# Optimization experiments

Hardware: AMD Instinct MI355X
Metric: run time of the kernel (lower is better)

## Reference

```python
import jax, jax.numpy as jnp
import numpy as np

EMBED_DIM = 256
NUM_EMBED = 1024
COMMIT_COST = 0.25


def setup_inputs() -> dict:
    key = jax.random.key(0)
    kx, kc = jax.random.split(key)
    x = jax.random.normal(kx, (64, 32, 32, EMBED_DIM), dtype=jnp.float32)
    codebook = jax.random.normal(kc, (NUM_EMBED, EMBED_DIM), dtype=jnp.float32)
    return {"x": x, "codebook": codebook}


def reference(x, codebook):
    # flatten to [N, D]
    flat_x = x.reshape(-1, EMBED_DIM)
    distances = (
        jnp.sum(flat_x ** 2, axis=1, keepdims=True)
        + jnp.sum(codebook ** 2, axis=1)
        - 2.0 * jnp.matmul(flat_x, codebook.T)
    )
    encoding_indices = jnp.argmin(distances, axis=1)  # [N]
    quantized = codebook[encoding_indices].reshape(x.shape)
    # losses (detach semantics via stop_gradient)
    q_latent_loss = jnp.mean((quantized - jax.lax.stop_gradient(x)) ** 2)
    e_latent_loss = jnp.mean((x - jax.lax.stop_gradient(quantized)) ** 2)
    loss = q_latent_loss + COMMIT_COST * e_latent_loss
    # straight-through estimator
    quantized = x + jax.lax.stop_gradient(quantized - x)
    return (quantized, loss)
```

## Files before the change

kernel.cpp:

```cpp
#include <hip/hip_runtime.h>

#define D 256
#define K 1024
#define NVEC 65536
#define ROWS 64
#define GROUPC 256
#define NG (K / GROUPC)
#define NKB (D / 32)
#define MARGIN 0.5f
#define MAXC 12
#define MAXP (ROWS * MAXC)

typedef __attribute__((ext_vector_type(8))) __bf16 bf16x8;
typedef __attribute__((ext_vector_type(4))) float floatx4;

__device__ inline unsigned short f2bf(float f) {
    unsigned int u = __float_as_uint(f);
    unsigned int r = u + 0x7fffu + ((u >> 16) & 1u);
    return (unsigned short)(r >> 16);
}
__device__ inline unsigned int fkey(float f) {
    unsigned int b = __float_as_uint(f);
    return (b & 0x80000000u) ? ~b : (b | 0x80000000u);
}
__device__ inline float unfkey(unsigned int k) {
    unsigned int b = (k & 0x80000000u) ? (k & 0x7fffffffu) : ~k;
    return __uint_as_float(b);
}


__global__ void vq_prep(const float* __restrict__ cb, float* __restrict__ cnorm,
                        unsigned short* __restrict__ cbf, float* __restrict__ lossAcc) {
    const int c = blockIdx.x;
    const int l = threadIdx.x;
    float4 v = *(const float4*)&cb[c * D + l * 4];
    float s = v.x * v.x + v.y * v.y + v.z * v.z + v.w * v.w;
#pragma unroll
    for (int off = 32; off > 0; off >>= 1) s += __shfl_down(s, off, 64);
    if (l == 0) cnorm[c] = s;
    const int g = c >> 8, w = (c >> 6) & 3, j = (c >> 4) & 3, col = c & 15;
    const int kb = l >> 3, quad = (l >> 1) & 3, h = (l & 1) * 4;
    const int S = ((g * 8 + kb) * 4 + w) * 4 + j;
    *(ushort4*)(cbf + (size_t)S * 512 + (quad * 16 + col) * 8 + h) =
        make_ushort4(f2bf(v.x), f2bf(v.y), f2bf(v.z), f2bf(v.w));
    if (c == 0 && l == 0) *lossAcc = 0.f;
}

__global__ __launch_bounds__(256, 4) void vq_fused(
        const float* __restrict__ x, const float* __restrict__ cb,
        const unsigned short* __restrict__ cbf, const float* __restrict__ cnorm,
        float* __restrict__ lossAcc, float* __restrict__ out)
{
    __shared__ __align__(16) unsigned short xs[ROWS * D];
    __shared__ unsigned int rowMinU[ROWS];
    __shared__ unsigned long long rowBest[ROWS];
    __shared__ int ccnt[ROWS];
    __shared__ int cand[ROWS][MAXC];
    __shared__ int pairs[MAXP];
    __shared__ int pcnt;
    __shared__ int widx[ROWS];
    __shared__ float wsum[4];

    const int tid = threadIdx.x;
    const int wave = tid >> 6;
    const int lane = tid & 63;
    const int quad = lane >> 4;
    const int col  = lane & 15;
    const int rowBase = blockIdx.x * ROWS;
    const float* xblk = x + (size_t)rowBase * D;

    if (tid < ROWS) { rowMinU[tid] = 0xFFFFFFFFu; rowBest[tid] = ~0ull; ccnt[tid] = 0; }
    if (tid == 0) pcnt = 0;

#pragma unroll
    for (int it = 0; it < 16; ++it) {
        int e = tid + it * 256;
        int r = e >> 6;
        int d4 = (e & 63) << 2;
        float4 v = *(const float4*)&xblk[r * D + d4];
        int slot = (d4 >> 3) ^ (r & 31);
        *(ushort4*)&xs[r * D + slot * 8 + (d4 & 4)] =
            make_ushort4(f2bf(v.x), f2bf(v.y), f2bf(v.z), f2bf(v.w));
    }
    __syncthreads();

    for (int g = 0; g < NG; ++g) {
        floatx4 acc[4][4];
#pragma unroll
        for (int i = 0; i < 4; ++i)
#pragma unroll
            for (int j = 0; j < 4; ++j) acc[i][j] = (floatx4){0.f, 0.f, 0.f, 0.f};

#pragma unroll
        for (int kb = 0; kb < NKB; ++kb) {
            bf16x8 af[4], bfr[4];
#pragma unroll
            for (int i = 0; i < 4; ++i) {
                int r = i * 16 + col;
                int slot = (kb * 4 + quad) ^ (r & 31);
                af[i] = *(const bf16x8*)&xs[r * D + slot * 8];
            }
#pragma unroll
            for (int j = 0; j < 4; ++j) {
                int S = ((g * 8 + kb) * 4 + wave) * 4 + j;
                bfr[j] = *(const bf16x8*)(cbf + (size_t)S * 512 + lane * 8);
            }
#pragma unroll
            for (int j = 0; j < 4; ++j)
#pragma unroll
                for (int i = 0; i < 4; ++i)
                    acc[i][j] = __builtin_amdgcn_mfma_f32_16x16x32_bf16(af[i], bfr[j], acc[i][j], 0, 0, 0);
        }

        const int cbase = g * GROUPC + wave * 64;
        float cn[4];
#pragma unroll
        for (int j = 0; j < 4; ++j) cn[j] = cnorm[cbase + j * 16 + col];

#pragma unroll
        for (int i = 0; i < 4; ++i)
#pragma unroll
            for (int reg = 0; reg < 4; ++reg) {
                float v = cn[0] - 2.f * acc[i][0][reg];
#pragma unroll
                for (int j = 1; j < 4; ++j)
                    v = fminf(v, cn[j] - 2.f * acc[i][j][reg]);
#pragma unroll
                for (int off = 1; off < 16; off <<= 1)
                    v = fminf(v, __shfl_xor(v, off, 64));
                if (col == 0)
                    atomicMin(&rowMinU[i * 16 + quad * 4 + reg], fkey(v));
            }
        __syncthreads();
#pragma unroll
        for (int i = 0; i < 4; ++i)
#pragma unroll
            for (int reg = 0; reg < 4; ++reg) {
                int row = i * 16 + quad * 4 + reg;
                float lim = unfkey(rowMinU[row]) + MARGIN;
#pragma unroll
                for (int j = 0; j < 4; ++j) {
                    float d2 = cn[j] - 2.f * acc[i][j][reg];
                    if (d2 < lim) {
                        int slot = atomicAdd(&ccnt[row], 1);
                        if (slot < MAXC) cand[row][slot] = cbase + j * 16 + col;
                    }
                }
            }
    }
    __syncthreads();

    if (tid < ROWS) {
        int m = ccnt[tid]; if (m > MAXC) m = MAXC;
        for (int c = 0; c < m; ++c) {
            int p = atomicAdd(&pcnt, 1);
            pairs[p] = (tid << 10) | cand[tid][c];
        }
    }
    __syncthreads();
    const int np = pcnt;

    const int team = wave * 4 + quad;
    for (int p = team; p < np; p += 16) {
        int pr = pairs[p];
        int row = pr >> 10, code = pr & 1023;
        const float* xr = xblk + row * D + col * 16;
        const float* er = cb + (size_t)code * D + col * 16;
        float s = 0.f;
#pragma unroll
        for (int q = 0; q < 4; ++q) {
            float4 a = *(const float4*)(xr + q * 4);
            float4 b = *(const float4*)(er + q * 4);
            s += a.x * b.x + a.y * b.y + a.z * b.z + a.w * b.w;
        }
#pragma unroll
        for (int off = 1; off < 16; off <<= 1) s += __shfl_xor(s, off, 64);
        if (col == 0) {
            float dist = cnorm[code] - 2.f * s;
            unsigned long long pack = ((unsigned long long)fkey(dist) << 32) | (unsigned int)code;
            atomicMin(&rowBest[row], pack);
        }
    }

    for (int rr = 0; rr < 16; ++rr) {
        const int rl = wave * 16 + rr;
        if (ccnt[rl] > MAXC) {
            float best = 3.4e38f;
            int bi = 0x7fffffff;
            for (int c = lane; c < K; c += 64) {
                float p = 0.f;
                for (int k = 0; k < D; ++k) p += xblk[rl * D + k] * cb[(size_t)c * D + k];
                float dist = cnorm[c] - 2.f * p;
                if (dist < best || (dist == best && c < bi)) { best = dist; bi = c; }
            }
#pragma unroll
            for (int off = 1; off < 64; off <<= 1) {
                float ob = __shfl_xor(best, off, 64);
                int oi = __shfl_xor(bi, off, 64);
                if (ob < best || (ob == best && oi < bi)) { best = ob; bi = oi; }
            }
            if (lane == 0)
                atomicMin(&rowBest[rl], ((unsigned long long)fkey(best) << 32) | (unsigned int)bi);
        }
    }
    __syncthreads();
    if (tid < ROWS) widx[tid] = (int)(rowBest[tid] & 0xffffffffu);
    __syncthreads();

    float part = 0.f;
#pragma unroll
    for (int it = 0; it < 16; ++it) {
        int e4 = tid + it * 256;
        int r = e4 >> 6, d4 = (e4 & 63) * 4;
        float4 q = *(const float4*)&cb[(size_t)widx[r] * D + d4];
        float4 xv = *(const float4*)&xblk[r * D + d4];
        *(float4*)&out[(size_t)rowBase * D + r * D + d4] = q;
        float a = q.x - xv.x, b = q.y - xv.y, c2 = q.z - xv.z, d2 = q.w - xv.w;
        part += a * a + b * b + c2 * c2 + d2 * d2;
    }
#pragma unroll
    for (int off = 32; off > 0; off >>= 1) part += __shfl_down(part, off, 64);
    if (lane == 0) wsum[wave] = part;
    __syncthreads();
    if (tid == 0) atomicAdd(lossAcc, wsum[0] + wsum[1] + wsum[2] + wsum[3]);
}

__global__ void vq_final_kernel(const float* __restrict__ lossAcc, float* __restrict__ outLoss) {
    *outLoss = 1.25f * (*lossAcc) / 16777216.f;
}

extern "C" void kernel_launch(void* const* d_in, const int* in_sizes, int n_in,
                              void* d_out, int out_size, void* d_ws, size_t ws_size,
                              hipStream_t stream) {
    const float* x  = (const float*)d_in[0];
    const float* cb = (const float*)d_in[1];
    float* out = (float*)d_out;

    float* cnorm = (float*)d_ws;
    float* lossAcc = cnorm + K;
    unsigned short* cbf = (unsigned short*)((char*)d_ws + 8192);

    vq_prep<<<K, 64, 0, stream>>>(cb, cnorm, cbf, lossAcc);
    vq_fused<<<NVEC / ROWS, 256, 0, stream>>>(x, cb, cbf, cnorm, lossAcc, out);
    vq_final_kernel<<<1, 1, 0, stream>>>(lossAcc, out + (size_t)NVEC * D);
}
```

Measured before the change: 244.7 us.

## Halve rows per block, flatten candidate list, compute loss from bf16 smem copy

Cuts the rows per block from 64 to 32 and raises the launch-bounds occupancy target from 4 to 6 blocks so more waves are resident. Candidate collection now appends straight into one shared pairs list, replacing per-row buckets plus a compaction pass. If that list overflows, the whole block falls back to a brute-force search. The loss now uses the bf16-rounded x held in shared memory instead of re-reading fp32 x from global memory, which changes its precision.

```diff
diff --git a/kernel.cpp b/kernel.cpp
--- a/kernel.cpp
+++ b/kernel.cpp
@@ -3,13 +3,12 @@
 #define D 256
 #define K 1024
 #define NVEC 65536
-#define ROWS 64
+#define ROWS 32
 #define GROUPC 256
 #define NG (K / GROUPC)
 #define NKB (D / 32)
 #define MARGIN 0.5f
-#define MAXC 12
-#define MAXP (ROWS * MAXC)
+#define MAXP 384
 
 typedef __attribute__((ext_vector_type(8))) __bf16 bf16x8;
 typedef __attribute__((ext_vector_type(4))) float floatx4;
@@ -19,6 +18,9 @@
     unsigned int r = u + 0x7fffu + ((u >> 16) & 1u);
     return (unsigned short)(r >> 16);
 }
+__device__ inline float bf2f(unsigned short h) {
+    return __uint_as_float((unsigned int)h << 16);
+}
 __device__ inline unsigned int fkey(float f) {
     unsigned int b = __float_as_uint(f);
     return (b & 0x80000000u) ? ~b : (b | 0x80000000u);
@@ -27,7 +29,6 @@
     unsigned int b = (k & 0x80000000u) ? (k & 0x7fffffffu) : ~k;
     return __uint_as_float(b);
 }
-
 
 __global__ void vq_prep(const float* __restrict__ cb, float* __restrict__ cnorm,
                         unsigned short* __restrict__ cbf, float* __restrict__ lossAcc) {
@@ -46,7 +47,7 @@
     if (c == 0 && l == 0) *lossAcc = 0.f;
 }
 
-__global__ __launch_bounds__(256, 4) void vq_fused(
+__global__ __launch_bounds__(256, 6) void vq_fused(
         const float* __restrict__ x, const float* __restrict__ cb,
         const unsigned short* __restrict__ cbf, const float* __restrict__ cnorm,
         float* __restrict__ lossAcc, float* __restrict__ out)
@@ -54,8 +55,6 @@
     __shared__ __align__(16) unsigned short xs[ROWS * D];
     __shared__ unsigned int rowMinU[ROWS];
     __shared__ unsigned long long rowBest[ROWS];
-    __shared__ int ccnt[ROWS];
-    __shared__ int cand[ROWS][MAXC];
     __shared__ int pairs[MAXP];
     __shared__ int pcnt;
     __shared__ int widx[ROWS];
@@ -69,35 +68,35 @@
     const int rowBase = blockIdx.x * ROWS;
     const float* xblk = x + (size_t)rowBase * D;
 
-    if (tid < ROWS) { rowMinU[tid] = 0xFFFFFFFFu; rowBest[tid] = ~0ull; ccnt[tid] = 0; }
+    if (tid < ROWS) { rowMinU[tid] = 0xFFFFFFFFu; rowBest[tid] = ~0ull; }
     if (tid == 0) pcnt = 0;
 
 #pragma unroll
-    for (int it = 0; it < 16; ++it) {
+    for (int it = 0; it < 8; ++it) {
         int e = tid + it * 256;
         int r = e >> 6;
         int d4 = (e & 63) << 2;
         float4 v = *(const float4*)&xblk[r * D + d4];
-        int slot = (d4 >> 3) ^ (r & 31);
+        int slot = (d4 >> 3) ^ r;
         *(ushort4*)&xs[r * D + slot * 8 + (d4 & 4)] =
             make_ushort4(f2bf(v.x), f2bf(v.y), f2bf(v.z), f2bf(v.w));
     }
     __syncthreads();
 
     for (int g = 0; g < NG; ++g) {
-        floatx4 acc[4][4];
-#pragma unroll
-        for (int i = 0; i < 4; ++i)
+        floatx4 acc[2][4];
+#pragma unroll
+        for (int i = 0; i < 2; ++i)
 #pragma unroll
             for (int j = 0; j < 4; ++j) acc[i][j] = (floatx4){0.f, 0.f, 0.f, 0.f};
 
 #pragma unroll
         for (int kb = 0; kb < NKB; ++kb) {
-            bf16x8 af[4], bfr[4];
-#pragma unroll
-            for (int i = 0; i < 4; ++i) {
+            bf16x8 af[2], bfr[4];
+#pragma unroll
+            for (int i = 0; i < 2; ++i) {
                 int r = i * 16 + col;
-                int slot = (kb * 4 + quad) ^ (r & 31);
+                int slot = (kb * 4 + quad) ^ r;
                 af[i] = *(const bf16x8*)&xs[r * D + slot * 8];
             }
 #pragma unroll
@@ -108,7 +107,7 @@
 #pragma unroll
             for (int j = 0; j < 4; ++j)
 #pragma unroll
-                for (int i = 0; i < 4; ++i)
+                for (int i = 0; i < 2; ++i)
                     acc[i][j] = __builtin_amdgcn_mfma_f32_16x16x32_bf16(af[i], bfr[j], acc[i][j], 0, 0, 0);
         }
 
@@ -118,7 +117,7 @@
         for (int j = 0; j < 4; ++j) cn[j] = cnorm[cbase + j * 16 + col];
 
 #pragma unroll
-        for (int i = 0; i < 4; ++i)
+        for (int i = 0; i < 2; ++i)
 #pragma unroll
             for (int reg = 0; reg < 4; ++reg) {
                 float v = cn[0] - 2.f * acc[i][0][reg];
@@ -133,7 +132,7 @@
             }
         __syncthreads();
 #pragma unroll
-        for (int i = 0; i < 4; ++i)
+        for (int i = 0; i < 2; ++i)
 #pragma unroll
             for (int reg = 0; reg < 4; ++reg) {
                 int row = i * 16 + quad * 4 + reg;
@@ -142,49 +141,40 @@
                 for (int j = 0; j < 4; ++j) {
                     float d2 = cn[j] - 2.f * acc[i][j][reg];
                     if (d2 < lim) {
-                        int slot = atomicAdd(&ccnt[row], 1);
-                        if (slot < MAXC) cand[row][slot] = cbase + j * 16 + col;
+                        int p = atomicAdd(&pcnt, 1);
+                        if (p < MAXP) pairs[p] = (row << 10) | (cbase + j * 16 + col);
                     }
                 }
             }
     }
     __syncthreads();
-
-    if (tid < ROWS) {
-        int m = ccnt[tid]; if (m > MAXC) m = MAXC;
-        for (int c = 0; c < m; ++c) {
-            int p = atomicAdd(&pcnt, 1);
-            pairs[p] = (tid << 10) | cand[tid][c];
+    const int np = pcnt;
+
+    if (np <= MAXP) {
+        const int team = wave * 4 + quad;
+        for (int p = team; p < np; p += 16) {
+            int pr = pairs[p];
+            int row = pr >> 10, code = pr & 1023;
+            const float* xr = xblk + row * D + col * 16;
+            const float* er = cb + (size_t)code * D + col * 16;
+            float s = 0.f;
+#pragma unroll
+            for (int q = 0; q < 4; ++q) {
+                float4 a = *(const float4*)(xr + q * 4);
+                float4 b = *(const float4*)(er + q * 4);
+                s += a.x * b.x + a.y * b.y + a.z * b.z + a.w * b.w;
+            }
+#pragma unroll
+            for (int off = 1; off < 16; off <<= 1) s += __shfl_xor(s, off, 64);
+            if (col == 0) {
+                float dist = cnorm[code] - 2.f * s;
+                atomicMin(&rowBest[row],
+                          ((unsigned long long)fkey(dist) << 32) | (unsigned int)code);
+            }
         }
-    }
-    __syncthreads();
-    const int np = pcnt;
-
-    const int team = wave * 4 + quad;
-    for (int p = team; p < np; p += 16) {
-        int pr = pairs[p];
-        int row = pr >> 10, code = pr & 1023;
-        const float* xr = xblk + row * D + col * 16;
-        const float* er = cb + (size_t)code * D + col * 16;
-        float s = 0.f;
-#pragma unroll
-        for (int q = 0; q < 4; ++q) {
-            float4 a = *(const float4*)(xr + q * 4);
-            float4 b = *(const float4*)(er + q * 4);
-            s += a.x * b.x + a.y * b.y + a.z * b.z + a.w * b.w;
-        }
-#pragma unroll
-        for (int off = 1; off < 16; off <<= 1) s += __shfl_xor(s, off, 64);
-        if (col == 0) {
-            float dist = cnorm[code] - 2.f * s;
-            unsigned long long pack = ((unsigned long long)fkey(dist) << 32) | (unsigned int)code;
-            atomicMin(&rowBest[row], pack);
-        }
-    }
-
-    for (int rr = 0; rr < 16; ++rr) {
-        const int rl = wave * 16 + rr;
-        if (ccnt[rl] > MAXC) {
+    } else {
+        for (int rr = 0; rr < 8; ++rr) {
+            const int rl = wave * 8 + rr;
             float best = 3.4e38f;
             int bi = 0x7fffffff;
             for (int c = lane; c < K; c += 64) {
@@ -209,13 +199,15 @@
 
     float part = 0.f;
 #pragma unroll
-    for (int it = 0; it < 16; ++it) {
+    for (int it = 0; it < 8; ++it) {
         int e4 = tid + it * 256;
         int r = e4 >> 6, d4 = (e4 & 63) * 4;
         float4 q = *(const float4*)&cb[(size_t)widx[r] * D + d4];
-        float4 xv = *(const float4*)&xblk[r * D + d4];
+        int slot = (d4 >> 3) ^ r;
+        ushort4 xh = *(const ushort4*)&xs[r * D + slot * 8 + (d4 & 4)];
         *(float4*)&out[(size_t)rowBase * D + r * D + d4] = q;
-        float a = q.x - xv.x, b = q.y - xv.y, c2 = q.z - xv.z, d2 = q.w - xv.w;
+        float a = q.x - bf2f(xh.x), b = q.y - bf2f(xh.y);
+        float c2 = q.z - bf2f(xh.z), d2 = q.w - bf2f(xh.w);
         part += a * a + b * b + c2 * c2 + d2 * d2;
     }
 #pragma unroll
```

Measured after the change: 263.2 us. +7.5%, slower.
